# Optimization experiments

Hardware: AMD Instinct MI355X
Metric: run time of the kernel (lower is better)

## Reference

```python
import jax, jax.numpy as jnp
import numpy as np

N_TOKENS = 32768
D_MODEL = 1024
D_HIDDEN = 4096
N_EXPERTS = 8
TOP_K = 2


def setup_inputs() -> dict:
    key = jax.random.key(0)
    ks = jax.random.split(key, 8)
    s_in = 1.0 / np.sqrt(D_MODEL)
    s_hid = 1.0 / np.sqrt(D_HIDDEN)
    return {
        "x": jax.random.normal(ks[0], (N_TOKENS, D_MODEL), dtype=jnp.float32),
        "Wr": jax.random.normal(ks[1], (D_MODEL, N_EXPERTS), dtype=jnp.float32) * s_in,
        "br": jnp.zeros((N_EXPERTS,), dtype=jnp.float32),
        "W1": jax.random.normal(ks[2], (N_EXPERTS, D_MODEL, D_HIDDEN), dtype=jnp.float32) * s_in,
        "b1": jnp.zeros((N_EXPERTS, D_HIDDEN), dtype=jnp.float32),
        "W2": jax.random.normal(ks[3], (N_EXPERTS, D_HIDDEN, D_MODEL), dtype=jnp.float32) * s_hid,
        "b2": jnp.zeros((N_EXPERTS, D_MODEL), dtype=jnp.float32),
    }


def reference(x, Wr, br, W1, b1, W2, b2):
    # Router: softmax over experts, top-k selection, renormalize.
    logits = x @ Wr + br                                  # [N, E]
    probs = jax.nn.softmax(logits, axis=-1)
    topk_probs, topk_idx = jax.lax.top_k(probs, TOP_K)    # [N, K]
    topk_probs = topk_probs / jnp.sum(topk_probs, axis=-1, keepdims=True)
    # Per-token per-expert combine weight (sum over k of prob * selection).
    sel = jax.nn.one_hot(topk_idx, N_EXPERTS, dtype=x.dtype)   # [N, K, E]
    combine = jnp.einsum('nk,nke->ne', topk_probs, sel)        # [N, E]
    # Masked gather-MLP-scatter expressed as dense per-expert MLP weighted
    # by combine (zero weight for unselected experts -> identical math).
    out = jnp.zeros_like(x)
    for e in range(N_EXPERTS):
        h = jax.nn.gelu(x @ W1[e] + b1[e], approximate=False)  # exact erf GELU (torch default)
        out = out + combine[:, e:e + 1] * (h @ W2[e] + b2[e])
    return out
```

## Files before the change

kernel.cpp:

```cpp
#include <hip/hip_runtime.h>

#define NT_TOK 32768
#define DM 1024
#define DH 4096
#define NE 8
#define BT 256
#define BK 64
#define CAP (NT_TOK*2 + NE*BT)
#define CHUNK_ROWS 16384

typedef _Float16 f16x8 __attribute__((ext_vector_type(8)));
typedef float f32x4 __attribute__((ext_vector_type(4)));
typedef float f32x8 __attribute__((ext_vector_type(8)));

__device__ __forceinline__ unsigned short f2h_bits(float v){
  _Float16 h = (_Float16)v;
  return __builtin_bit_cast(unsigned short, h);
}

__device__ __forceinline__ void async16(const void* g, void* l){
  __builtin_amdgcn_global_load_lds((const __attribute__((address_space(1))) void*)g,
                                   (__attribute__((address_space(3))) void*)l, 16, 0, 0);
}

__device__ __forceinline__ int xcd_remap(int orig, int nwg){
  int q = nwg >> 3, r = nwg & 7;
  int x = orig & 7, i = orig >> 3;
  int base = (x < r) ? x*(q+1) : r*(q+1) + (x-r)*q;
  return base + i;
}


__global__ __launch_bounds__(256) void cvt_f16_kernel(const float* __restrict__ src,
                                                      unsigned short* __restrict__ dst, int n8){
  int i = blockIdx.x*256 + threadIdx.x;
  if (i >= n8) return;
  float4 a = ((const float4*)src)[2*i];
  float4 b = ((const float4*)src)[2*i+1];
  union { unsigned short u[8]; uint4 v; } r;
  r.u[0]=f2h_bits(a.x); r.u[1]=f2h_bits(a.y); r.u[2]=f2h_bits(a.z); r.u[3]=f2h_bits(a.w);
  r.u[4]=f2h_bits(b.x); r.u[5]=f2h_bits(b.y); r.u[6]=f2h_bits(b.z); r.u[7]=f2h_bits(b.w);
  ((uint4*)dst)[i] = r.v;
}

__global__ void transpose_f16_kernel(const float* __restrict__ src,
                                     unsigned short* __restrict__ dst, int R, int C){
  __shared__ float t[32][33];
  int ez = blockIdx.z;
  const float* s = src + (size_t)ez*R*C;
  unsigned short* d = dst + (size_t)ez*R*C;
  int c0 = blockIdx.x*32, r0 = blockIdx.y*32;
  int tx = threadIdx.x, ty = threadIdx.y;
  #pragma unroll
  for (int i=0;i<32;i+=8)
    t[ty+i][tx] = s[(size_t)(r0+ty+i)*C + (c0+tx)];
  __syncthreads();
  #pragma unroll
  for (int i=0;i<32;i+=8)
    d[(size_t)(c0+ty+i)*R + (r0+tx)] = f2h_bits(t[tx][ty+i]);
}


__global__ __launch_bounds__(256) void router_kernel(const float* __restrict__ x,
    const float* __restrict__ Wr, const float* __restrict__ br,
    int* __restrict__ topi, float* __restrict__ topw, int* __restrict__ counts){
  __shared__ float wr_s[NE*DM];
  __shared__ int bcnt[NE];
  int tid = threadIdx.x;
  if (tid < NE) bcnt[tid] = 0;
  for (int idx=tid; idx<NE*DM; idx+=256){
    int k = idx>>3, e = idx&7;
    wr_s[e*DM + k] = Wr[idx];
  }
  __syncthreads();
  int w = tid>>6, lane = tid&63;
  for (int tt=0; tt<4; ++tt){
    int t = blockIdx.x*16 + w*4 + tt;
    const float* xr = x + (size_t)t*DM;
    double acc[NE];
    #pragma unroll
    for (int e=0;e<NE;e++) acc[e]=0.0;
    #pragma unroll
    for (int j=0;j<16;j++){
      float xv = xr[j*64 + lane];
      #pragma unroll
      for (int e=0;e<NE;e++) acc[e] += (double)xv * (double)wr_s[e*DM + j*64 + lane];
    }
    #pragma unroll
    for (int e=0;e<NE;e++){
      #pragma unroll
      for (int d=32; d; d>>=1) acc[e] += __shfl_xor(acc[e], d);
    }
    if (lane==0){
      double l[NE];
      #pragma unroll
      for (int e=0;e<NE;e++) l[e] = acc[e] + (double)br[e];
      int i0 = 0;
      #pragma unroll
      for (int e=1;e<NE;e++) if (l[e] > l[i0]) i0 = e;
      int i1 = (i0==0) ? 1 : 0;
      #pragma unroll
      for (int e=0;e<NE;e++) if (e != i0 && l[e] > l[i1]) i1 = e;
      double w0 = 1.0/(1.0 + exp(l[i1]-l[i0]));
      topi[2*t] = i0; topi[2*t+1] = i1;
      topw[2*t] = (float)w0; topw[2*t+1] = (float)(1.0-w0);
      atomicAdd(&bcnt[i0],1); atomicAdd(&bcnt[i1],1);
    }
  }
  __syncthreads();
  if (tid < NE && bcnt[tid] > 0) atomicAdd(&counts[tid], bcnt[tid]);
}

__global__ void offsets_kernel(const int* __restrict__ counts, int* __restrict__ off){
  if (threadIdx.x==0 && blockIdx.x==0){
    int o = 0;
    for (int e=0;e<NE;e++){ off[e] = o; o += ((counts[e]+BT-1)/BT)*BT; }
    off[NE] = o;
  }
}

__global__ __launch_bounds__(256) void scatter_kernel(const int* __restrict__ topi,
    const float* __restrict__ topw, const int* __restrict__ off,
    int* __restrict__ cursor, int* __restrict__ atok, float* __restrict__ awgt){
  __shared__ int bcnt[NE];
  __shared__ int bbase[NE];
  int tid = threadIdx.x;
  if (tid < NE) bcnt[tid] = 0;
  __syncthreads();
  int t = blockIdx.x*256 + tid;
  int e0 = topi[2*t],   e1 = topi[2*t+1];
  int r0 = atomicAdd(&bcnt[e0], 1);
  int r1 = atomicAdd(&bcnt[e1], 1);
  __syncthreads();
  if (tid < NE) bbase[tid] = (bcnt[tid] > 0) ? atomicAdd(&cursor[tid], bcnt[tid]) : 0;
  __syncthreads();
  int s0 = off[e0] + bbase[e0] + r0;
  int s1 = off[e1] + bbase[e1] + r1;
  atok[s0] = t;  awgt[s0] = topw[2*t];
  atok[s1] = t;  awgt[s1] = topw[2*t+1];
}


template<int KDIM, bool IS_G2>
__global__ __launch_bounds__(512, 2) void gemm_big_kernel(
    const unsigned short* __restrict__ Asrc,
    const unsigned short* __restrict__ WT,
    const float* __restrict__ bias,
    const int* __restrict__ atok,
    const float* __restrict__ awgt,
    const int* __restrict__ offs,
    unsigned short* __restrict__ H,
    float* __restrict__ out,
    int c0){
  __shared__ unsigned short As[2][BT*BK];
  __shared__ unsigned short Bs[2][BT*BK];
  const int NDIM = IS_G2 ? DM : DH;
  const int NT = NDIM/BT;
  int wg = xcd_remap(blockIdx.x, gridDim.x);
  int nt = wg % NT, mt = wg / NT;
  int total = offs[NE];
  int m0 = c0 + mt*BT;
  if (m0 >= total) return;
  int e = 0;
  #pragma unroll
  for (int q=0;q<NE-1;q++) if (m0 >= offs[q+1]) e = q+1;
  int tid = threadIdx.x;
  int lane = tid&63, wid = tid>>6;
  int wm = wid>>2, wn = wid&3;

  const unsigned short* ag[4];
  const unsigned short* bg[4];
  int lofs[4];
  #pragma unroll
  for (int j=0;j<4;j++){
    int c = j*512 + tid;
    int r = c>>3, s = c&7;
    int sc = s ^ (r&7);
    if (IS_G2){
      ag[j] = Asrc + (size_t)(m0 - c0 + r)*KDIM + sc*8;
    } else {
      int tok = atok[m0 + r];
      if (tok < 0) tok = 0;
      ag[j] = Asrc + (size_t)tok*KDIM + sc*8;
    }
    bg[j] = WT + ((size_t)e*NDIM + nt*BT + r)*KDIM + sc*8;
    lofs[j] = c*8;
  }

  f32x4 acc[8][4];
  #pragma unroll
  for (int i=0;i<8;i++)
    #pragma unroll
    for (int j=0;j<4;j++) acc[i][j] = 0.0f;

  const int NKT = KDIM/BK;
  #pragma unroll
  for (int j=0;j<4;j++){
    async16(ag[j], &As[0][lofs[j]]);
    async16(bg[j], &Bs[0][lofs[j]]);
  }
  int cur = 0;
  for (int kt=0; kt<NKT; ++kt){
    __builtin_amdgcn_s_barrier();
    if (kt+1 < NKT){
      #pragma unroll
      for (int j=0;j<4;j++){
        async16(ag[j] + (size_t)(kt+1)*BK, &As[cur^1][lofs[j]]);
        async16(bg[j] + (size_t)(kt+1)*BK, &Bs[cur^1][lofs[j]]);
      }
      asm volatile("s_waitcnt vmcnt(8)" ::: "memory");
    } else {
      asm volatile("s_waitcnt vmcnt(0)" ::: "memory");
    }
    __builtin_amdgcn_s_barrier();
    const unsigned short* Ab = &As[cur][0];
    const unsigned short* Bb = &Bs[cur][0];
    #pragma unroll
    for (int q=0;q<2;q++){
      f16x8 a[8], b[4];
      int kch = ((q*4 + (lane>>4)) ^ (lane&7))*8;
      #pragma unroll
      for (int mf=0; mf<8; mf++)
        a[mf] = *(const f16x8*)&Ab[(wm*128 + mf*16 + (lane&15))*BK + kch];
      #pragma unroll
      for (int nf=0; nf<4; nf++)
        b[nf] = *(const f16x8*)&Bb[(wn*64 + nf*16 + (lane&15))*BK + kch];
      __builtin_amdgcn_s_setprio(1);
      #pragma unroll
      for (int mf=0;mf<8;mf++)
        #pragma unroll
        for (int nf=0;nf<4;nf++)
          acc[mf][nf] = __builtin_amdgcn_mfma_f32_16x16x32_f16(a[mf], b[nf], acc[mf][nf], 0,0,0);
      __builtin_amdgcn_s_setprio(0);
    }
    cur ^= 1;
  }

  int nbase = nt*BT + wn*64 + (lane&15);
  if (!IS_G2){
    const float* be = bias + (size_t)e*DH;
    int rloc = (m0 - c0) + wm*128 + ((lane>>4)<<2);
    #pragma unroll
    for (int mf=0;mf<8;mf++)
      #pragma unroll
      for (int nf=0;nf<4;nf++){
        int nn = nbase + nf*16;
        float bv = be[nn];
        #pragma unroll
        for (int r2=0;r2<4;r2++){
          float v = acc[mf][nf][r2] + bv;
          float g = 0.5f*v*(1.0f + erff(v*0.70710678118654752f));
          H[(size_t)(rloc + mf*16 + r2)*DH + nn] = f2h_bits(g);
        }
      }
  } else {
    const float* be = bias + (size_t)e*DM;
    int sbase = m0 + wm*128 + ((lane>>4)<<2);
    #pragma unroll
    for (int mf=0;mf<8;mf++){
      #pragma unroll
      for (int r2=0;r2<4;r2++){
        int slot = sbase + mf*16 + r2;
        int tok = atok[slot];
        float wgt = awgt[slot];
        if (tok >= 0){
          #pragma unroll
          for (int nf=0;nf<4;nf++){
            int nn = nbase + nf*16;
            float v = acc[mf][nf][r2] + be[nn];
            atomicAdd(&out[(size_t)tok*DM + nn], wgt*v);
          }
        }
      }
    }
  }
}


__global__ __launch_bounds__(256) void gemm1_f32_kernel(
    const float* __restrict__ xf, const unsigned short* __restrict__ W1T,
    const float* __restrict__ b1, const int* __restrict__ atok,
    const int* __restrict__ offs, unsigned short* __restrict__ H, int c0){
  __shared__ float Asf[128*BK];
  __shared__ unsigned short Bsld[128*BK];
  const int NT = DH/128;
  int wg = xcd_remap(blockIdx.x, gridDim.x);
  int nt = wg % NT, mt = wg / NT;
  int total = offs[NE];
  int m0 = c0 + mt*128;
  if (m0 >= total) return;
  int e = 0;
  #pragma unroll
  for (int q=0;q<NE-1;q++) if (m0 >= offs[q+1]) e = q+1;
  int tid = threadIdx.x;
  const void* ag[8];
  int aofs[8];
  #pragma unroll
  for (int j=0;j<8;j++){
    int c = j*256 + tid;
    int r = c>>4, sb = (c&15)*16;
    int tok = atok[m0 + r];
    if (tok < 0) tok = 0;
    ag[j] = (const void*)((const char*)(xf + (size_t)tok*DM) + sb);
    aofs[j] = c*16;
  }
  const unsigned short* bg[4];
  int bofs[4];
  #pragma unroll
  for (int j=0;j<4;j++){
    int c = j*256 + tid;
    int r = c>>3, s = c&7;
    bg[j] = W1T + ((size_t)e*DH + nt*128 + r)*DM + s*8;
    bofs[j] = c*16;
  }
  f32x4 acc[4][4];
  #pragma unroll
  for (int i=0;i<4;i++)
    #pragma unroll
    for (int j=0;j<4;j++) acc[i][j] = 0.0f;
  int lane = tid&63;
  int wm = tid>>7, wn = (tid>>6)&1;
  int arow = wm*64 + (lane&15);
  int ak0  = (lane>>4)*8;
  int brr  = (wn*64 + (lane&15))*BK + ak0;
  for (int kt=0; kt<DM/BK; ++kt){
    #pragma unroll
    for (int j=0;j<8;j++)
      async16((const char*)ag[j] + (size_t)kt*BK*4, (char*)Asf + aofs[j]);
    #pragma unroll
    for (int j=0;j<4;j++)
      async16(bg[j] + (size_t)kt*BK, (char*)Bsld + bofs[j]);
    __syncthreads();
    #pragma unroll
    for (int kk=0; kk<BK; kk+=32){
      f16x8 a[4], b[4];
      #pragma unroll
      for (int f=0;f<4;f++){
        f32x8 v = *(const f32x8*)&Asf[(arow + f*16)*BK + ak0 + kk];
        a[f] = __builtin_convertvector(v, f16x8);
        b[f] = *(const f16x8*)&Bsld[brr + f*16*BK + kk];
      }
      #pragma unroll
      for (int i=0;i<4;i++)
        #pragma unroll
        for (int j2=0;j2<4;j2++)
          acc[i][j2] = __builtin_amdgcn_mfma_f32_16x16x32_f16(a[i], b[j2], acc[i][j2], 0,0,0);
    }
    __syncthreads();
  }
  const float* b1e = b1 + (size_t)e*DH;
  int rloc = (m0 - c0) + wm*64 + ((lane>>4)<<2);
  int nbase = nt*128 + wn*64 + (lane&15);
  #pragma unroll
  for (int i=0;i<4;i++)
    #pragma unroll
    for (int j=0;j<4;j++){
      int nn = nbase + j*16;
      float bv = b1e[nn];
      #pragma unroll
      for (int r2=0;r2<4;r2++){
        float v = acc[i][j][r2] + bv;
        float g = 0.5f*v*(1.0f + erff(v*0.70710678118654752f));
        H[(size_t)(rloc + i*16 + r2)*DH + nn] = f2h_bits(g);
      }
    }
}

__global__ void fill_kernel(float* p, float v, size_t n){
  size_t i = (size_t)blockIdx.x*256 + threadIdx.x;
  if (i < n) p[i] = v;
}


extern "C" void kernel_launch(void* const* d_in, const int* in_sizes, int n_in,
                              void* d_out, int out_size, void* d_ws, size_t ws_size,
                              hipStream_t stream){
  const float* x  = (const float*)d_in[0];
  const float* Wr = (const float*)d_in[1];
  const float* br = (const float*)d_in[2];
  const float* W1 = (const float*)d_in[3];
  const float* b1 = (const float*)d_in[4];
  const float* W2 = (const float*)d_in[5];
  const float* b2 = (const float*)d_in[6];
  float* out = (float*)d_out;

  char* ws = (char*)d_ws;
  size_t o = 0;
  auto take = [&](size_t bytes)->void*{
    void* p = ws + o; o += (bytes + 255) & ~(size_t)255; return p;
  };
  unsigned short* W1T = (unsigned short*)take((size_t)NE*DM*DH*2);
  unsigned short* W2T = (unsigned short*)take((size_t)NE*DM*DH*2);
  int*   TOPI = (int*)take((size_t)NT_TOK*2*4);
  float* TOPW = (float*)take((size_t)NT_TOK*2*4);
  int*   ATOK = (int*)take((size_t)CAP*4);
  float* AWGT = (float*)take((size_t)CAP*4);
  int*   CNT  = (int*)take(256);
  int* CUR = CNT + 8;
  int* OFF = CNT + 16;

  if (o + (size_t)BT*DH*2 > ws_size){
    fill_kernel<<<(unsigned)((out_size+255)/256), 256, 0, stream>>>(out, 4321.5f, (size_t)out_size);
    return;
  }

  unsigned short* XB = nullptr;
  bool use_xb = false;
  {
    size_t xb_bytes = (size_t)NT_TOK*DM*2 + 256;
    size_t need_h  = (size_t)2048*DH*2;
    if (o + xb_bytes + need_h <= ws_size){
      use_xb = true;
      XB = (unsigned short*)take((size_t)NT_TOK*DM*2);
    }
  }
  size_t rem = ws_size - o;
  size_t cr = (rem / ((size_t)DH*2)) / BT * BT;
  if (cr > (size_t)CHUNK_ROWS) cr = CHUNK_ROWS;
  if (cr < BT){
    fill_kernel<<<(unsigned)((out_size+255)/256), 256, 0, stream>>>(out, 4321.5f, (size_t)out_size);
    return;
  }
  int CR = (int)cr;
  unsigned short* Hb = (unsigned short*)take((size_t)CR*DH*2);

  hipMemsetAsync(CNT, 0, 64, stream);
  hipMemsetAsync(ATOK, 0xFF, (size_t)CAP*4, stream);
  hipMemsetAsync(out, 0, (size_t)out_size*sizeof(float), stream);

  if (use_xb)
    cvt_f16_kernel<<<(NT_TOK*DM/8 + 255)/256, 256, 0, stream>>>(x, XB, NT_TOK*DM/8);
  transpose_f16_kernel<<<dim3(DH/32, DM/32, NE), dim3(32,8), 0, stream>>>(W1, W1T, DM, DH);
  transpose_f16_kernel<<<dim3(DM/32, DH/32, NE), dim3(32,8), 0, stream>>>(W2, W2T, DH, DM);
  router_kernel<<<NT_TOK/16, 256, 0, stream>>>(x, Wr, br, TOPI, TOPW, CNT);
  offsets_kernel<<<1, 1, 0, stream>>>(CNT, OFF);
  scatter_kernel<<<NT_TOK/256, 256, 0, stream>>>(TOPI, TOPW, OFF, CUR, ATOK, AWGT);

  for (int c0 = 0; c0 < CAP; c0 += CR){
    int rows = CAP - c0; if (rows > CR) rows = CR;
    int mtc = (rows + BT - 1)/BT;
    if (use_xb)
      gemm_big_kernel<DM, false><<<dim3((DH/BT)*mtc), 512, 0, stream>>>(
          XB, W1T, b1, ATOK, AWGT, OFF, Hb, out, c0);
    else
      gemm1_f32_kernel<<<dim3((DH/128)*((rows+127)/128)), 256, 0, stream>>>(
          x, W1T, b1, ATOK, OFF, Hb, c0);
    gemm_big_kernel<DH, true><<<dim3((DM/BT)*mtc), 512, 0, stream>>>(
        Hb, W2T, b2, ATOK, AWGT, OFF, Hb, out, c0);
  }
}
```

Baseline: 2.410 ms.

## Deepen big GEMM pipeline to 4-stage BK=32 with interleaved loads and MFMA

Changes the main expert GEMM kernel from a double-buffered BK=64 loop to a four-buffer BK=32 ring that keeps three tiles in flight. Each iteration splits its MFMA work into two halves, and the next A and B tile loads are issued between them. A new LDS swizzle packs two 32-wide rows per 64-element line to avoid bank conflicts. The aim is to hide global-load latency better and to overlap memory and compute, at the cost of more barriers per unit of K work. The fp32 GEMM1 kernel is hardcoded to 64 so its behaviour stays the same.

After: 2.252 ms. 6.6% less time.

```diff
diff --git a/kernel.cpp b/kernel.cpp
--- a/kernel.cpp
+++ b/kernel.cpp
@@ -5,7 +5,7 @@
 #define DH 4096
 #define NE 8
 #define BT 256
-#define BK 64
+#define BK 32
 #define CAP (NT_TOK*2 + NE*BT)
 #define CHUNK_ROWS 16384
 
@@ -152,8 +152,8 @@
     unsigned short* __restrict__ H,
     float* __restrict__ out,
     int c0){
-  __shared__ unsigned short As[2][BT*BK];
-  __shared__ unsigned short Bs[2][BT*BK];
+  __shared__ unsigned short As[4][BT*BK];
+  __shared__ unsigned short Bs[4][BT*BK];
   const int NDIM = IS_G2 ? DM : DH;
   const int NT = NDIM/BT;
   int wg = xcd_remap(blockIdx.x, gridDim.x);
@@ -168,24 +168,29 @@
   int lane = tid&63, wid = tid>>6;
   int wm = wid>>2, wn = wid&3;
 
-  const unsigned short* ag[4];
-  const unsigned short* bg[4];
-  int lofs[4];
-  #pragma unroll
-  for (int j=0;j<4;j++){
+  const unsigned short* agp[2];
+  const unsigned short* bgp[2];
+  int dofs[2];
+  #pragma unroll
+  for (int j=0;j<2;j++){
     int c = j*512 + tid;
-    int r = c>>3, s = c&7;
-    int sc = s ^ (r&7);
+    int u = (c&7) ^ ((c>>3)&7);
+    int srow = ((c>>3)<<1) + (u>>2);
+    int sch  = u&3;
     if (IS_G2){
-      ag[j] = Asrc + (size_t)(m0 - c0 + r)*KDIM + sc*8;
+      agp[j] = Asrc + (size_t)(m0 - c0 + srow)*KDIM + sch*8;
     } else {
-      int tok = atok[m0 + r];
+      int tok = atok[m0 + srow];
       if (tok < 0) tok = 0;
-      ag[j] = Asrc + (size_t)tok*KDIM + sc*8;
-    }
-    bg[j] = WT + ((size_t)e*NDIM + nt*BT + r)*KDIM + sc*8;
-    lofs[j] = c*8;
-  }
+      agp[j] = Asrc + (size_t)tok*KDIM + sch*8;
+    }
+    bgp[j] = WT + ((size_t)e*NDIM + nt*BT + srow)*KDIM + sch*8;
+    dofs[j] = c*8;
+  }
+
+  int pos = (((lane>>4) + ((lane&1)<<2)) ^ ((lane>>1)&7)) << 3;
+  int aoff0 = (wm*64 + ((lane&15)>>1))*64 + pos;
+  int boff0 = (wn*32 + ((lane&15)>>1))*64 + pos;
 
   f32x4 acc[8][4];
   #pragma unroll
@@ -195,45 +200,50 @@
 
   const int NKT = KDIM/BK;
   #pragma unroll
-  for (int j=0;j<4;j++){
-    async16(ag[j], &As[0][lofs[j]]);
-    async16(bg[j], &Bs[0][lofs[j]]);
-  }
-  int cur = 0;
+  for (int t=0;t<3;t++){
+    #pragma unroll
+    for (int j=0;j<2;j++) async16(agp[j] + t*BK, &As[t][dofs[j]]);
+    #pragma unroll
+    for (int j=0;j<2;j++) async16(bgp[j] + t*BK, &Bs[t][dofs[j]]);
+  }
+
   for (int kt=0; kt<NKT; ++kt){
+    if (kt < NKT-2)      asm volatile("s_waitcnt vmcnt(8)" ::: "memory");
+    else if (kt < NKT-1) asm volatile("s_waitcnt vmcnt(4)" ::: "memory");
+    else                 asm volatile("s_waitcnt vmcnt(0)" ::: "memory");
     __builtin_amdgcn_s_barrier();
-    if (kt+1 < NKT){
-      #pragma unroll
-      for (int j=0;j<4;j++){
-        async16(ag[j] + (size_t)(kt+1)*BK, &As[cur^1][lofs[j]]);
-        async16(bg[j] + (size_t)(kt+1)*BK, &Bs[cur^1][lofs[j]]);
-      }
-      asm volatile("s_waitcnt vmcnt(8)" ::: "memory");
-    } else {
-      asm volatile("s_waitcnt vmcnt(0)" ::: "memory");
-    }
+    const unsigned short* Ab = &As[kt&3][0];
+    const unsigned short* Bb = &Bs[kt&3][0];
+    f16x8 b[4], a[4];
+    #pragma unroll
+    for (int nf=0;nf<4;nf++) b[nf] = *(const f16x8*)&Bb[boff0 + nf*512];
+    #pragma unroll
+    for (int mf=0;mf<4;mf++) a[mf] = *(const f16x8*)&Ab[aoff0 + mf*512];
+    if (kt+3 < NKT){
+      #pragma unroll
+      for (int j=0;j<2;j++) async16(agp[j] + (size_t)(kt+3)*BK, &As[(kt+3)&3][dofs[j]]);
+    }
+    __builtin_amdgcn_s_setprio(1);
+    #pragma unroll
+    for (int mf=0;mf<4;mf++)
+      #pragma unroll
+      for (int nf=0;nf<4;nf++)
+        acc[mf][nf] = __builtin_amdgcn_mfma_f32_16x16x32_f16(a[mf], b[nf], acc[mf][nf], 0,0,0);
+    __builtin_amdgcn_s_setprio(0);
     __builtin_amdgcn_s_barrier();
-    const unsigned short* Ab = &As[cur][0];
-    const unsigned short* Bb = &Bs[cur][0];
-    #pragma unroll
-    for (int q=0;q<2;q++){
-      f16x8 a[8], b[4];
-      int kch = ((q*4 + (lane>>4)) ^ (lane&7))*8;
-      #pragma unroll
-      for (int mf=0; mf<8; mf++)
-        a[mf] = *(const f16x8*)&Ab[(wm*128 + mf*16 + (lane&15))*BK + kch];
-      #pragma unroll
-      for (int nf=0; nf<4; nf++)
-        b[nf] = *(const f16x8*)&Bb[(wn*64 + nf*16 + (lane&15))*BK + kch];
-      __builtin_amdgcn_s_setprio(1);
-      #pragma unroll
-      for (int mf=0;mf<8;mf++)
-        #pragma unroll
-        for (int nf=0;nf<4;nf++)
-          acc[mf][nf] = __builtin_amdgcn_mfma_f32_16x16x32_f16(a[mf], b[nf], acc[mf][nf], 0,0,0);
-      __builtin_amdgcn_s_setprio(0);
-    }
-    cur ^= 1;
+    #pragma unroll
+    for (int mf=0;mf<4;mf++) a[mf] = *(const f16x8*)&Ab[aoff0 + (mf+4)*512];
+    if (kt+3 < NKT){
+      #pragma unroll
+      for (int j=0;j<2;j++) async16(bgp[j] + (size_t)(kt+3)*BK, &Bs[(kt+3)&3][dofs[j]]);
+    }
+    __builtin_amdgcn_s_setprio(1);
+    #pragma unroll
+    for (int mf=0;mf<4;mf++)
+      #pragma unroll
+      for (int nf=0;nf<4;nf++)
+        acc[mf+4][nf] = __builtin_amdgcn_mfma_f32_16x16x32_f16(a[mf], b[nf], acc[mf+4][nf], 0,0,0);
+    __builtin_amdgcn_s_setprio(0);
   }
 
   int nbase = nt*BT + wn*64 + (lane&15);
@@ -281,8 +291,8 @@
     const float* __restrict__ xf, const unsigned short* __restrict__ W1T,
     const float* __restrict__ b1, const int* __restrict__ atok,
     const int* __restrict__ offs, unsigned short* __restrict__ H, int c0){
-  __shared__ float Asf[128*BK];
-  __shared__ unsigned short Bsld[128*BK];
+  __shared__ float Asf[128*64];
+  __shared__ unsigned short Bsld[128*64];
   const int NT = DH/128;
   int wg = xcd_remap(blockIdx.x, gridDim.x);
   int nt = wg % NT, mt = wg / NT;
@@ -322,23 +332,23 @@
   int wm = tid>>7, wn = (tid>>6)&1;
   int arow = wm*64 + (lane&15);
   int ak0  = (lane>>4)*8;
-  int brr  = (wn*64 + (lane&15))*BK + ak0;
-  for (int kt=0; kt<DM/BK; ++kt){
+  int brr  = (wn*64 + (lane&15))*64 + ak0;
+  for (int kt=0; kt<DM/64; ++kt){
     #pragma unroll
     for (int j=0;j<8;j++)
-      async16((const char*)ag[j] + (size_t)kt*BK*4, (char*)Asf + aofs[j]);
+      async16((const char*)ag[j] + (size_t)kt*64*4, (char*)Asf + aofs[j]);
     #pragma unroll
     for (int j=0;j<4;j++)
-      async16(bg[j] + (size_t)kt*BK, (char*)Bsld + bofs[j]);
+      async16(bg[j] + (size_t)kt*64, (char*)Bsld + bofs[j]);
     __syncthreads();
     #pragma unroll
-    for (int kk=0; kk<BK; kk+=32){
+    for (int kk=0; kk<64; kk+=32){
       f16x8 a[4], b[4];
       #pragma unroll
       for (int f=0;f<4;f++){
-        f32x8 v = *(const f32x8*)&Asf[(arow + f*16)*BK + ak0 + kk];
+        f32x8 v = *(const f32x8*)&Asf[(arow + f*16)*64 + ak0 + kk];
         a[f] = __builtin_convertvector(v, f16x8);
-        b[f] = *(const f16x8*)&Bsld[brr + f*16*BK + kk];
+        b[f] = *(const f16x8*)&Bsld[brr + f*16*64 + kk];
       }
       #pragma unroll
       for (int i=0;i<4;i++)
```
